# Kernel tuning notes

Measured on AMD Instinct MI355X. Metric: run time of the kernel, lower is better.

Reference implementation:

```python
import jax, jax.numpy as jnp
import numpy as np

CONCENTRATION_WEIGHT = 1.0


def setup_inputs() -> dict:
    key = jax.random.key(0)
    k1, k2 = jax.random.split(key)
    pred = jax.random.normal(k1, (16, 10, 512, 512), dtype=jnp.float32)
    target = jax.random.uniform(k2, (16, 10, 512, 512), dtype=jnp.float32)
    return {"pred": pred, "target": target}


def reference(pred, target):
    # pred, target: [B, C, H, W]
    B, C, H, W = pred.shape
    y = jnp.arange(H, dtype=pred.dtype)[:, None]   # [H,1]
    x = jnp.arange(W, dtype=pred.dtype)[None, :]   # [1,W]

    mass = target.sum(axis=(2, 3))                 # [B,C]
    valid = mass > 0                               # [B,C] bool
    safe_mass = jnp.where(valid, mass, jnp.ones_like(mass))

    # masked centroids per (b,c)
    cy = (target * y).sum(axis=(2, 3)) / safe_mass  # [B,C]
    cx = (target * x).sum(axis=(2, 3)) / safe_mass  # [B,C]

    # squared distance field per (b,c): [B,C,H,W]
    dist_sq = (y[None, None, :, :] - cy[:, :, None, None]) ** 2 \
            + (x[None, None, :, :] - cx[:, :, None, None]) ** 2

    per_slice = jnp.mean(jax.nn.sigmoid(pred) * dist_sq, axis=(2, 3))  # [B,C]

    n_valid = valid.sum()
    loss_sum = jnp.where(valid, per_slice, jnp.zeros_like(per_slice)).sum()
    loss = jnp.where(n_valid > 0,
                     loss_sum / jnp.maximum(n_valid, 1).astype(pred.dtype),
                     jnp.asarray(0.0, dtype=pred.dtype))
    return loss * CONCENTRATION_WEIGHT
```

## Files before the change

### kernel.cpp

```cpp
#include <hip/hip_runtime.h>


#define HW 262144
#define F4_SLICE 65536
#define SLICES 160
#define NBLK 2048
#define V4B 5120
#define GROUPS 5
#define THREADS 256
#define NACC 8

__global__ __launch_bounds__(THREADS) void conc_pass1(
    const float* __restrict__ pred,
    const float* __restrict__ target,
    float* __restrict__ ws) {
  const int b = blockIdx.x;
  const int tid = threadIdx.x;
  const int start4 = b * V4B;
  const int lane = tid & 63, wave = tid >> 6;

  const float4* __restrict__ p4 = reinterpret_cast<const float4*>(pred);
  const float4* __restrict__ t4 = reinterpret_cast<const float4*>(target);

  float T0 = 0.f, T1 = 0.f, T2 = 0.f, T3 = 0.f, Ty = 0.f;
  float G0 = 0.f, G1 = 0.f, G2 = 0.f, G3 = 0.f, Gy = 0.f, Gyy = 0.f;

  const float x0c = (float)((tid & 127) << 2);

  __shared__ float red[4][NACC];

#define FLUSH(REC)                                                        \
  {                                                                       \
    const float x1c = x0c + 1.f, x2c = x0c + 2.f, x3c = x0c + 3.f;        \
    float acc[NACC];                                                      \
    acc[0] = (T0 + T1) + (T2 + T3);                                       \
    acc[1] = Ty;                                                          \
    acc[2] = (T0 * x0c + T1 * x1c) + (T2 * x2c + T3 * x3c);               \
    acc[3] = (G0 + G1) + (G2 + G3);                                       \
    acc[4] = Gy;                                                          \
    acc[5] = (G0 * x0c + G1 * x1c) + (G2 * x2c + G3 * x3c);               \
    acc[6] = Gyy;                                                         \
    acc[7] = (G0 * (x0c * x0c) + G1 * (x1c * x1c)) +                      \
             (G2 * (x2c * x2c) + G3 * (x3c * x3c));                       \
    _Pragma("unroll") for (int k = 0; k < NACC; ++k) {                    \
      float v = acc[k];                                                   \
      _Pragma("unroll") for (int off = 32; off > 0; off >>= 1)            \
          v += __shfl_down(v, off, 64);                                   \
      acc[k] = v;                                                         \
    }                                                                     \
    if (lane == 0) {                                                      \
      _Pragma("unroll") for (int k = 0; k < NACC; ++k)                    \
          red[wave][k] = acc[k];                                          \
    }                                                                     \
    __syncthreads();                                                      \
    if (tid < NACC)                                                       \
      ws[(size_t)(b * 2 + (REC)) * NACC + tid] =                          \
          red[0][tid] + red[1][tid] + red[2][tid] + red[3][tid];          \
    __syncthreads();                                                      \
    T0 = T1 = T2 = T3 = Ty = 0.f;                                         \
    G0 = G1 = G2 = G3 = Gy = Gyy = 0.f;                                   \
  }

  const int off_in_slice = start4 & (F4_SLICE - 1);
  const bool crosses = (off_in_slice + V4B) > F4_SLICE;
  const int cg = crosses ? ((F4_SLICE - off_in_slice) >> 10) : GROUPS;

  for (int g = 0; g < GROUPS; ++g) {
    if (g == cg) FLUSH(0);
    const int g4 = start4 + g * 1024;
    const float yg = (float)(((g4 & (F4_SLICE - 1)) >> 7) + (tid >> 7));
    float4 tb[4], pb[4];
#pragma unroll
    for (int k = 0; k < 4; ++k) {
      const int v4 = g4 + k * THREADS + tid;
      tb[k] = t4[v4];
      pb[k] = p4[v4];
    }
#pragma unroll
    for (int k = 0; k < 4; ++k) {
      const float y = yg + (float)(2 * k);
      const float4 t = tb[k];
      const float4 p = pb[k];

      T0 += t.x; T1 += t.y; T2 += t.z; T3 += t.w;
      const float ts = (t.x + t.y) + (t.z + t.w);
      Ty += ts * y;

      const float g0 = 1.f / (1.f + __expf(-p.x));
      const float g1 = 1.f / (1.f + __expf(-p.y));
      const float g2 = 1.f / (1.f + __expf(-p.z));
      const float g3 = 1.f / (1.f + __expf(-p.w));
      G0 += g0; G1 += g1; G2 += g2; G3 += g3;
      const float gs = (g0 + g1) + (g2 + g3);
      const float gsy = gs * y;
      Gy  += gsy;
      Gyy += gsy * y;
    }
  }

  if (crosses) {
    FLUSH(1);
  } else {
    FLUSH(0);
    if (tid < NACC) ws[(size_t)(b * 2 + 1) * NACC + tid] = 0.f;
  }
#undef FLUSH
}

__global__ __launch_bounds__(THREADS) void conc_pass2(
    const float* __restrict__ ws, float* __restrict__ out) {
  const int tid = threadIdx.x;
  double lsum = 0.0;
  int nvalid = 0;

  if (tid < SLICES) {
    const int s = tid;
    float a[NACC];
#pragma unroll
    for (int k = 0; k < NACC; ++k) a[k] = 0.f;

    const int blo = (s * F4_SLICE) / V4B;
    const int bhi = ((s + 1) * F4_SLICE - 1) / V4B;
    for (int b = blo; b <= bhi; ++b) {
      const int first_slice = (b * V4B) >> 16;
      const int rec = (first_slice == s) ? 0 : 1;
      const float4* r =
          reinterpret_cast<const float4*>(ws + (size_t)(b * 2 + rec) * NACC);
      const float4 lo = r[0], hi = r[1];
      a[0] += lo.x; a[1] += lo.y; a[2] += lo.z; a[3] += lo.w;
      a[4] += hi.x; a[5] += hi.y; a[6] += hi.z; a[7] += hi.w;
    }

    const double tm = a[0], ty = a[1], tx = a[2];
    const double m0 = a[3], msy = a[4], msx = a[5], syy = a[6], sxx = a[7];
    const bool valid = tm > 0.0;
    const double mass = valid ? tm : 1.0;
    const double cy = ty / mass, cx = tx / mass;
    const double conc =
        syy + sxx - 2.0 * cy * msy - 2.0 * cx * msx + (cy * cy + cx * cx) * m0;
    if (valid) {
      lsum = conc / (double)HW;
      nvalid = 1;
    }
  }

  const int lane = tid & 63, wave = tid >> 6;
  double v = lsum;
  int n = nvalid;
#pragma unroll
  for (int off = 32; off > 0; off >>= 1) {
    v += __shfl_down(v, off, 64);
    n += __shfl_down(n, off, 64);
  }
  __shared__ double sd[4];
  __shared__ int si[4];
  if (lane == 0) { sd[wave] = v; si[wave] = n; }
  __syncthreads();
  if (tid == 0) {
    const double t = sd[0] + sd[1] + sd[2] + sd[3];
    const int nn = si[0] + si[1] + si[2] + si[3];
    out[0] = (float)((nn > 0) ? (t / (double)nn) : 0.0);
  }
}

extern "C" void kernel_launch(void* const* d_in, const int* in_sizes, int n_in,
                              void* d_out, int out_size, void* d_ws, size_t ws_size,
                              hipStream_t stream) {
  const float* pred = (const float*)d_in[0];
  const float* target = (const float*)d_in[1];
  float* ws = (float*)d_ws;
  float* out = (float*)d_out;

  conc_pass1<<<NBLK, THREADS, 0, stream>>>(pred, target, ws);
  conc_pass2<<<1, THREADS, 0, stream>>>(ws, out);
}
```

Baseline: 67.23 us.

## Double-buffer pass1 input tiles through LDS using async global_load_lds

Pass 1 now streams pred and target through a two-stage LDS ring filled with global_load_lds, in 512-float4 tiles, instead of loading 4 float4s per tensor into registers per group. The load of the next tile is issued before computing the current one, and explicit vmcnt waits order the two. Each wave only reads LDS slots it filled itself, so no block barrier is needed. The aim is more bytes in flight and less VGPR pressure on this bandwidth-bound reduction. The cost is extra LDS traffic and reliance on hand-written waitcnt counts.

Result: no change. 67.75 us (+0.8%).

```diff
diff --git a/kernel.cpp b/kernel.cpp
--- a/kernel.cpp
+++ b/kernel.cpp
@@ -1,4 +1,5 @@
 #include <hip/hip_runtime.h>
+#include <stdint.h>
 
 
 #define HW 262144
@@ -6,9 +7,17 @@
 #define SLICES 160
 #define NBLK 2048
 #define V4B 5120
-#define GROUPS 5
+#define T4 512
+#define NT (V4B / T4)
 #define THREADS 256
 #define NACC 8
+
+#define AS1 __attribute__((address_space(1)))
+#define AS3 __attribute__((address_space(3)))
+
+__device__ __forceinline__ void gl_lds16(const float4* g, float4* l) {
+  __builtin_amdgcn_global_load_lds((AS1 void*)g, (AS3 void*)l, 16, 0, 0);
+}
 
 __global__ __launch_bounds__(THREADS) void conc_pass1(
     const float* __restrict__ pred,
@@ -22,12 +31,13 @@
   const float4* __restrict__ p4 = reinterpret_cast<const float4*>(pred);
   const float4* __restrict__ t4 = reinterpret_cast<const float4*>(target);
 
+  __shared__ float4 lds[2][2][T4];
+  __shared__ float red[4][NACC];
+
   float T0 = 0.f, T1 = 0.f, T2 = 0.f, T3 = 0.f, Ty = 0.f;
   float G0 = 0.f, G1 = 0.f, G2 = 0.f, G3 = 0.f, Gy = 0.f, Gyy = 0.f;
 
   const float x0c = (float)((tid & 127) << 2);
-
-  __shared__ float red[4][NACC];
 
 #define FLUSH(REC)                                                        \
   {                                                                       \
@@ -61,26 +71,39 @@
     G0 = G1 = G2 = G3 = Gy = Gyy = 0.f;                                   \
   }
 
+  auto stage = [&](int i, int bf) {
+    const int g4 = start4 + i * T4;
+#pragma unroll
+    for (int k = 0; k < 2; ++k) {
+      const int off = k * 256 + wave * 64;
+      gl_lds16(t4 + g4 + off + lane, &lds[bf][0][off]);
+      gl_lds16(p4 + g4 + off + lane, &lds[bf][1][off]);
+    }
+  };
+
   const int off_in_slice = start4 & (F4_SLICE - 1);
   const bool crosses = (off_in_slice + V4B) > F4_SLICE;
-  const int cg = crosses ? ((F4_SLICE - off_in_slice) >> 10) : GROUPS;
+  const int ct = crosses ? ((F4_SLICE - off_in_slice) / T4) : NT;
 
-  for (int g = 0; g < GROUPS; ++g) {
-    if (g == cg) FLUSH(0);
-    const int g4 = start4 + g * 1024;
-    const float yg = (float)(((g4 & (F4_SLICE - 1)) >> 7) + (tid >> 7));
-    float4 tb[4], pb[4];
+  stage(0, 0);
+
+  for (int i = 0; i < NT; ++i) {
+    const int bf = i & 1;
+    if (i + 1 < NT) {
+      stage(i + 1, bf ^ 1);
+      asm volatile("s_waitcnt vmcnt(4)" ::: "memory");
+    } else {
+      asm volatile("s_waitcnt vmcnt(0)" ::: "memory");
+    }
+    if (i == ct) FLUSH(0);
+
+    const float yg =
+        (float)((((start4 + i * T4) & (F4_SLICE - 1)) >> 7) + (tid >> 7));
 #pragma unroll
-    for (int k = 0; k < 4; ++k) {
-      const int v4 = g4 + k * THREADS + tid;
-      tb[k] = t4[v4];
-      pb[k] = p4[v4];
-    }
-#pragma unroll
-    for (int k = 0; k < 4; ++k) {
+    for (int k = 0; k < 2; ++k) {
+      const float4 t = lds[bf][0][k * 256 + tid];
+      const float4 p = lds[bf][1][k * 256 + tid];
       const float y = yg + (float)(2 * k);
-      const float4 t = tb[k];
-      const float4 p = pb[k];
 
       T0 += t.x; T1 += t.y; T2 += t.z; T3 += t.w;
       const float ts = (t.x + t.y) + (t.z + t.w);
```
